# Performance work log

Measured on AMD Instinct MI355X. Metric: run time of the kernel, lower is better.

The kernel has to match this reference:

```python
import jax, jax.numpy as jnp
import numpy as np

DIM = 512
EPS = 1e-08
LN_EPS = 1e-05  # torch LayerNorm default


def layer_norm(x, g, b):
    mu = jnp.mean(x, axis=-1, keepdims=True)
    var = jnp.mean(jnp.square(x - mu), axis=-1, keepdims=True)
    return (x - mu) * jax.lax.rsqrt(var + LN_EPS) * g + b


def setup_inputs() -> dict:
    key = jax.random.key(0)
    ks = jax.random.split(key, 10)
    B, NQ, NK, D = 8, 1024, 2048, DIM
    s = 1.0 / np.sqrt(D)
    return {
        "inputs": jax.random.normal(ks[0], (B, NQ, D), jnp.float32),
        "context": jax.random.normal(ks[1], (B, NK, D), jnp.float32),
        "ln_in_g": jnp.ones((D,), jnp.float32),
        "ln_in_b": jnp.zeros((D,), jnp.float32),
        "ln_ctx_g": jnp.ones((D,), jnp.float32),
        "ln_ctx_b": jnp.zeros((D,), jnp.float32),
        "Wq": jax.random.uniform(ks[2], (D, D), jnp.float32, -s, s),
        "bq": jax.random.uniform(ks[3], (D,), jnp.float32, -s, s),
        "Wk": jax.random.uniform(ks[4], (D, D), jnp.float32, -s, s),
        "bk": jax.random.uniform(ks[5], (D,), jnp.float32, -s, s),
        "Wv": jax.random.uniform(ks[6], (D, D), jnp.float32, -s, s),
        "bv": jax.random.uniform(ks[7], (D,), jnp.float32, -s, s),
    }


def reference(inputs, context, ln_in_g, ln_in_b, ln_ctx_g, ln_ctx_b, Wq, bq, Wk, bk, Wv, bv):
    x = layer_norm(inputs, ln_in_g, ln_in_b)
    c = layer_norm(context, ln_ctx_g, ln_ctx_b)
    q = x @ Wq.T + bq  # [B, Nq, D]
    k = c @ Wk.T + bk  # [B, Nk, D]
    v = c @ Wv.T + bv  # [B, Nk, D]
    scale = DIM ** (-0.5)
    dots = jnp.einsum('bid,bjd->bij', q, k) * scale  # [B, Nq, Nk]
    attn = jax.nn.softmax(dots, axis=1) + EPS  # softmax over query axis
    attn = attn / jnp.sum(attn, axis=2, keepdims=True)  # renorm over key axis
    updates = jnp.einsum('bjd,bij->bid', v, attn)
    return updates
```

## Files before the change

kernel.cpp:

```cpp
#include <hip/hip_runtime.h>

using u16 = unsigned short;
typedef __attribute__((ext_vector_type(8))) short short8;
typedef __attribute__((ext_vector_type(4))) float floatx4;

#define NQ 1024
#define NK 2048
#define DD 512

__device__ __forceinline__ u16 f2bf(float f) {
  union { float f; unsigned u; } x; x.f = f;
  unsigned r = (x.u + 0x7fffu + ((x.u >> 16) & 1u)) >> 16;
  return (u16)r;
}
__device__ __forceinline__ float bf2f(u16 u) {
  union { unsigned u; float f; } x; x.u = ((unsigned)u) << 16; return x.f;
}
__device__ __forceinline__ float wave_sum(float v) {
#pragma unroll
  for (int off = 32; off > 0; off >>= 1) v += __shfl_down(v, off, 64);
  return v;
}
__device__ __forceinline__ void gload16(const u16* g, const u16* l) {
  __builtin_amdgcn_global_load_lds(
      (const __attribute__((address_space(1))) void*)g,
      (__attribute__((address_space(3))) void*)l, 16, 0, 0);
}

__global__ __launch_bounds__(256) void ln_prep(
    const float* __restrict__ X1, const float* __restrict__ G1,
    const float* __restrict__ B1, u16* __restrict__ Y1,
    const float* __restrict__ X2, const float* __restrict__ G2,
    const float* __restrict__ B2, u16* __restrict__ Y2,
    const float* __restrict__ Wq, const float* __restrict__ Wk,
    const float* __restrict__ Wv, u16* __restrict__ wqb,
    u16* __restrict__ wkb, u16* __restrict__ wvb, float* __restrict__ Zero) {
  const int bx = blockIdx.x;
  const int t = threadIdx.x;
  if (bx >= 6144) {
    int e = bx - 6144;
    if (e < 768) {
      const float* src = e < 256 ? Wq : (e < 512 ? Wk : Wv);
      u16* dst = e < 256 ? wqb : (e < 512 ? wkb : wvb);
      int i = ((e & 255) * 256 + t) * 4;
      float4 v = *(const float4*)(src + i);
      ushort4 o;
      o.x = f2bf(v.x); o.y = f2bf(v.y); o.z = f2bf(v.z); o.w = f2bf(v.w);
      *(ushort4*)(dst + i) = o;
    } else {
      int i = ((e - 768) * 256 + t) * 4;
      float4 z = {0.f, 0.f, 0.f, 0.f};
      *(float4*)(Zero + i) = z;
    }
    return;
  }
  const int wave = t >> 6, lane = t & 63;
  int row = bx * 4 + wave;
  const float *X, *G, *Bv; u16* Y;
  if (row < 8192) { X = X1; G = G1; Bv = B1; Y = Y1; }
  else { row -= 8192; X = X2; G = G2; Bv = B2; Y = Y2; }
  const float4* Xp = (const float4*)(X + (long)row * DD);
  float4 v0 = Xp[lane * 2], v1 = Xp[lane * 2 + 1];
  float s = v0.x + v0.y + v0.z + v0.w + v1.x + v1.y + v1.z + v1.w;
  float ss = v0.x * v0.x + v0.y * v0.y + v0.z * v0.z + v0.w * v0.w +
             v1.x * v1.x + v1.y * v1.y + v1.z * v1.z + v1.w * v1.w;
  s = wave_sum(s);  s = __shfl(s, 0, 64);
  ss = wave_sum(ss); ss = __shfl(ss, 0, 64);
  float mu = s * (1.f / DD);
  float var = ss * (1.f / DD) - mu * mu;
  float rs = rsqrtf(var + 1e-5f);
  const float4* Gp = (const float4*)G;
  const float4* Bp = (const float4*)Bv;
  float4 g0 = Gp[lane * 2], g1 = Gp[lane * 2 + 1];
  float4 b0 = Bp[lane * 2], b1 = Bp[lane * 2 + 1];
  short8 o;
  o[0] = (short)f2bf((v0.x - mu) * rs * g0.x + b0.x);
  o[1] = (short)f2bf((v0.y - mu) * rs * g0.y + b0.y);
  o[2] = (short)f2bf((v0.z - mu) * rs * g0.z + b0.z);
  o[3] = (short)f2bf((v0.w - mu) * rs * g0.w + b0.w);
  o[4] = (short)f2bf((v1.x - mu) * rs * g1.x + b1.x);
  o[5] = (short)f2bf((v1.y - mu) * rs * g1.y + b1.y);
  o[6] = (short)f2bf((v1.z - mu) * rs * g1.z + b1.z);
  o[7] = (short)f2bf((v1.w - mu) * rs * g1.w + b1.w);
  *(short8*)(Y + (long)row * DD + lane * 8) = o;
}

__global__ __launch_bounds__(256) void gemm_proj(
    const u16* __restrict__ A1, const u16* __restrict__ W1,
    const float* __restrict__ b1, u16* __restrict__ C1,
    const u16* __restrict__ A2, const u16* __restrict__ W2,
    const float* __restrict__ b2, u16* __restrict__ C2) {
  __shared__ u16 smem[16384];
  u16* lA = smem;
  u16* lB = smem + 8192;
  const u16 *A, *B; const float* bias; u16* Cout;
  int m0 = blockIdx.x * 128;
  if (blockIdx.x < 64) { A = A1; B = W1; bias = b1; Cout = C1; }
  else { A = A2; B = W2; bias = b2; Cout = C2; m0 = (blockIdx.x - 64) * 128; }
  const int n0 = blockIdx.y * 128;
  const int t = threadIdx.x, wave = t >> 6, lane = t & 63;
  const int fm = lane & 15, fq = lane >> 4;
  const int wm = (wave >> 1) * 64, wn = (wave & 1) * 64;

  const int srow = t >> 3;
  const int swz = ((t & 7) ^ (srow & 7)) * 8;
  const u16* gA = A + (long)(m0 + srow) * 512 + swz;
  const u16* gB = B + (long)(n0 + srow) * 512 + swz;
  u16* dA = lA + wave * 512;
  u16* dB = lB + wave * 512;

  floatx4 acc[4][4];
#pragma unroll
  for (int x = 0; x < 4; ++x)
#pragma unroll
    for (int y = 0; y < 4; ++y) { floatx4 z = {0.f, 0.f, 0.f, 0.f}; acc[x][y] = z; }

#pragma unroll 1
  for (int kt = 0; kt < 8; ++kt) {
    gload16(gA, dA);
    gload16(gA + 32L * 512, dA + 2048);
    gload16(gA + 64L * 512, dA + 4096);
    gload16(gA + 96L * 512, dA + 6144);
    gload16(gB, dB);
    gload16(gB + 32L * 512, dB + 2048);
    gload16(gB + 64L * 512, dB + 4096);
    gload16(gB + 96L * 512, dB + 6144);
    gA += 64; gB += 64;
    __syncthreads();
#pragma unroll
    for (int ks = 0; ks < 2; ++ks) {
      short8 af[4], bfr[4];
      const int csl = ((ks * 4 + fq) ^ (fm & 7)) * 8;
#pragma unroll
      for (int x = 0; x < 4; ++x)
        af[x] = *(const short8*)&lA[(wm + x * 16 + fm) * 64 + csl];
#pragma unroll
      for (int y = 0; y < 4; ++y)
        bfr[y] = *(const short8*)&lB[(wn + y * 16 + fm) * 64 + csl];
#pragma unroll
      for (int x = 0; x < 4; ++x)
#pragma unroll
        for (int y = 0; y < 4; ++y)
          acc[x][y] = __builtin_amdgcn_mfma_f32_16x16x32_bf16(af[x], bfr[y], acc[x][y], 0, 0, 0);
    }
    __syncthreads();
  }

  float bs[4];
#pragma unroll
  for (int y = 0; y < 4; ++y) bs[y] = bias[n0 + wn + y * 16 + fm];
#pragma unroll
  for (int x = 0; x < 4; ++x)
#pragma unroll
    for (int y = 0; y < 4; ++y) {
      const int cblk = (wn >> 4) + y;
#pragma unroll
      for (int r = 0; r < 4; ++r) {
        int rowl = wm + x * 16 + fq * 4 + r;
        smem[rowl * 128 + ((cblk ^ fq) * 16) + fm] = f2bf(acc[x][y][r] + bs[y]);
      }
    }
  __syncthreads();
#pragma unroll
  for (int p = 0; p < 8; ++p) {
    int rowl = p * 16 + (t >> 4);
    int c = t & 15;
    int q = (rowl >> 2) & 3;
    short8 v = *(const short8*)&smem[rowl * 128 + (((c >> 1) ^ q) * 16) + (c & 1) * 8];
    *(short8*)(Cout + (long)(m0 + rowl) * 512 + n0 + c * 8) = v;
  }
}

__global__ __launch_bounds__(256) void qk_vproj(
    const u16* __restrict__ qb, const u16* __restrict__ kb,
    u16* __restrict__ E, float* __restrict__ Z,
    const u16* __restrict__ wvb, const u16* __restrict__ cb,
    const float* __restrict__ bv, u16* __restrict__ vT,
    float* __restrict__ colV, float scale) {
  __shared__ u16 smem[16384];
  __shared__ float colred[128];
  u16* lA = smem;
  u16* lB = smem + 8192;

  const int bx = blockIdx.x;
  const bool is_qk = bx < 1024;
  const u16 *A, *B;
  int m0, n0, b;
  if (is_qk) {
    b = bx & 7;
    n0 = ((bx >> 3) & 15) * 128;
    m0 = (bx >> 7) * 128;
    A = qb + (long)b * (1024L * 512);
    B = kb + (long)b * (2048L * 512);
  } else {
    int e = bx - 1024;
    m0 = (e & 3) * 128;
    n0 = (e >> 2) * 128;
    b = 0;
    A = wvb;
    B = cb;
  }
  const int t = threadIdx.x, wave = t >> 6, lane = t & 63;
  const int fm = lane & 15, fq = lane >> 4;
  const int wm = (wave >> 1) * 64, wn = (wave & 1) * 64;

  const int srow = t >> 3;
  const int swz = ((t & 7) ^ (srow & 7)) * 8;
  const u16* gA = A + (long)(m0 + srow) * 512 + swz;
  const u16* gB = B + (long)(n0 + srow) * 512 + swz;
  u16* dA = lA + wave * 512;
  u16* dB = lB + wave * 512;

  floatx4 acc[4][4];
#pragma unroll
  for (int x = 0; x < 4; ++x)
#pragma unroll
    for (int y = 0; y < 4; ++y) { floatx4 z = {0.f, 0.f, 0.f, 0.f}; acc[x][y] = z; }

#pragma unroll 1
  for (int kt = 0; kt < 8; ++kt) {
    gload16(gA, dA);
    gload16(gA + 32L * 512, dA + 2048);
    gload16(gA + 64L * 512, dA + 4096);
    gload16(gA + 96L * 512, dA + 6144);
    gload16(gB, dB);
    gload16(gB + 32L * 512, dB + 2048);
    gload16(gB + 64L * 512, dB + 4096);
    gload16(gB + 96L * 512, dB + 6144);
    gA += 64; gB += 64;
    __syncthreads();
#pragma unroll
    for (int ks = 0; ks < 2; ++ks) {
      short8 af[4], bfr[4];
      const int csl = ((ks * 4 + fq) ^ (fm & 7)) * 8;
#pragma unroll
      for (int x = 0; x < 4; ++x)
        af[x] = *(const short8*)&lA[(wm + x * 16 + fm) * 64 + csl];
#pragma unroll
      for (int y = 0; y < 4; ++y)
        bfr[y] = *(const short8*)&lB[(wn + y * 16 + fm) * 64 + csl];
#pragma unroll
      for (int x = 0; x < 4; ++x)
#pragma unroll
        for (int y = 0; y < 4; ++y)
          acc[x][y] = __builtin_amdgcn_mfma_f32_16x16x32_bf16(af[x], bfr[y], acc[x][y], 0, 0, 0);
    }
    __syncthreads();
  }

  if (is_qk) {
    float s4[4] = {0.f, 0.f, 0.f, 0.f};
#pragma unroll
    for (int x = 0; x < 4; ++x)
#pragma unroll
      for (int y = 0; y < 4; ++y) {
        const int cblk = (wn >> 4) + y;
#pragma unroll
        for (int r = 0; r < 4; ++r) {
          int rowl = wm + x * 16 + fq * 4 + r;
          float e = __expf(acc[x][y][r] * scale);
          s4[y] += e;
          smem[rowl * 128 + ((cblk ^ fq) * 16) + fm] = f2bf(e);
        }
      }
#pragma unroll
    for (int y = 0; y < 4; ++y) {
      s4[y] += __shfl_xor(s4[y], 16, 64);
      s4[y] += __shfl_xor(s4[y], 32, 64);
    }
    if (t < 128) colred[t] = 0.f;
    __syncthreads();
    u16* Eg = E + (long)b * (1024L * 2048);
#pragma unroll
    for (int p = 0; p < 8; ++p) {
      int rowl = p * 16 + (t >> 4);
      int c = t & 15;
      int q = (rowl >> 2) & 3;
      short8 v = *(const short8*)&smem[rowl * 128 + (((c >> 1) ^ q) * 16) + (c & 1) * 8];
      *(short8*)(Eg + (long)(m0 + rowl) * 2048 + n0 + c * 8) = v;
    }
    if (fq == 0) {
#pragma unroll
      for (int y = 0; y < 4; ++y) atomicAdd(&colred[wn + y * 16 + fm], s4[y]);
    }
    __syncthreads();
    if (t < 128) atomicAdd(&Z[b * 2048 + n0 + t], colred[t]);
  } else {
    const int bb = n0 >> 11;
    const int j0c = n0 & 2047;
    float bsr[4][4];
#pragma unroll
    for (int x = 0; x < 4; ++x)
#pragma unroll
      for (int r = 0; r < 4; ++r)
        bsr[x][r] = bv[m0 + wm + x * 16 + fq * 4 + r];
    float rs[4][4];
#pragma unroll
    for (int x = 0; x < 4; ++x)
#pragma unroll
      for (int r = 0; r < 4; ++r) rs[x][r] = 0.f;
#pragma unroll
    for (int x = 0; x < 4; ++x)
#pragma unroll
      for (int y = 0; y < 4; ++y) {
        const int cblk = (wn >> 4) + y;
#pragma unroll
        for (int r = 0; r < 4; ++r) {
          int rowl = wm + x * 16 + fq * 4 + r;
          float val = acc[x][y][r] + bsr[x][r];
          rs[x][r] += val;
          smem[rowl * 128 + ((cblk ^ fq) * 16) + fm] = f2bf(val);
        }
      }
    __syncthreads();
    u16* Cg = vT + (long)bb * (512L * 2048) + j0c;
#pragma unroll
    for (int p = 0; p < 8; ++p) {
      int rowl = p * 16 + (t >> 4);
      int c = t & 15;
      int q = (rowl >> 2) & 3;
      short8 v = *(const short8*)&smem[rowl * 128 + (((c >> 1) ^ q) * 16) + (c & 1) * 8];
      *(short8*)(Cg + (long)(m0 + rowl) * 2048 + c * 8) = v;
    }
#pragma unroll
    for (int x = 0; x < 4; ++x)
#pragma unroll
      for (int r = 0; r < 4; ++r) {
        float s = rs[x][r];
        s += __shfl_xor(s, 1, 64);
        s += __shfl_xor(s, 2, 64);
        s += __shfl_xor(s, 4, 64);
        s += __shfl_xor(s, 8, 64);
        if (fm == 0)
          atomicAdd(&colV[bb * 512 + m0 + wm + x * 16 + fq * 4 + r], s);
      }
  }
}

__global__ __launch_bounds__(256) void scaleV(u16* __restrict__ vT,
                                              const float* __restrict__ Z) {
  const long f = ((long)blockIdx.x * 256 + threadIdx.x) * 8;
  const int b = (int)(f >> 20);
  const float* zp = Z + b * 2048 + (int)(f & 2047);
  short8 v = *(const short8*)(vT + f);
  short8 o;
#pragma unroll
  for (int k = 0; k < 8; ++k)
    o[k] = (short)f2bf(bf2f((u16)v[k]) * __builtin_amdgcn_rcpf(zp[k]));
  *(short8*)(vT + f) = o;
}

__global__ __launch_bounds__(256) void gemm_pv(const u16* __restrict__ E,
    const u16* __restrict__ V, const float* __restrict__ colV,
    const float* __restrict__ Z, float* __restrict__ out) {
  __shared__ u16 smem[8192];
  __shared__ u16 sZb[2048];
  u16* lA = smem;
  u16* lB = smem + 4096;
  const int id = blockIdx.x;
  const int b = id & 7;
  const int m0 = ((id >> 3) & 15) * 64, n0 = (id >> 7) * 64;
  const int t = threadIdx.x, wave = t >> 6, lane = t & 63;
  const int fm = lane & 15, fq = lane >> 4;
  const int wm = (wave >> 1) * 32, wn = (wave & 1) * 32;

  {
    int i = t * 8;
    float4 z0 = *(const float4*)(Z + b * 2048 + i);
    float4 z1 = *(const float4*)(Z + b * 2048 + i + 4);
    short8 o;
    o[0] = (short)f2bf(__builtin_amdgcn_rcpf(z0.x));
    o[1] = (short)f2bf(__builtin_amdgcn_rcpf(z0.y));
    o[2] = (short)f2bf(__builtin_amdgcn_rcpf(z0.z));
    o[3] = (short)f2bf(__builtin_amdgcn_rcpf(z0.w));
    o[4] = (short)f2bf(__builtin_amdgcn_rcpf(z1.x));
    o[5] = (short)f2bf(__builtin_amdgcn_rcpf(z1.y));
    o[6] = (short)f2bf(__builtin_amdgcn_rcpf(z1.z));
    o[7] = (short)f2bf(__builtin_amdgcn_rcpf(z1.w));
    *(short8*)&sZb[i] = o;
  }

  const int srow = t >> 3;
  const int swz = ((t & 7) ^ (srow & 7)) * 8;
  const u16* gA = E + (long)b * (1024L * 2048) + (long)(m0 + srow) * 2048 + swz;
  const u16* gB = V + (long)b * (512L * 2048) + (long)(n0 + srow) * 2048 + swz;
  u16* dA = lA + wave * 512;
  u16* dB = lB + wave * 512;

  floatx4 acc[2][2];
  floatx4 accR[2];
#pragma unroll
  for (int x = 0; x < 2; ++x) {
    floatx4 z = {0.f, 0.f, 0.f, 0.f};
    accR[x] = z;
#pragma unroll
    for (int y = 0; y < 2; ++y) acc[x][y] = z;
  }

#pragma unroll 1
  for (int kt = 0; kt < 32; ++kt) {
    gload16(gA, dA);
    gload16(gA + 32L * 2048, dA + 2048);
    gload16(gB, dB);
    gload16(gB + 32L * 2048, dB + 2048);
    gA += 64; gB += 64;
    __syncthreads();
#pragma unroll
    for (int ks = 0; ks < 2; ++ks) {
      short8 af[2], bfr[2];
      const int chunk = ks * 4 + fq;
      const int csl = (chunk ^ (fm & 7)) * 8;
#pragma unroll
      for (int x = 0; x < 2; ++x)
        af[x] = *(const short8*)&lA[(wm + x * 16 + fm) * 64 + csl];
#pragma unroll
      for (int y = 0; y < 2; ++y)
        bfr[y] = *(const short8*)&lB[(wn + y * 16 + fm) * 64 + csl];
      short8 zf = *(const short8*)&sZb[kt * 64 + chunk * 8];
#pragma unroll
      for (int x = 0; x < 2; ++x) {
#pragma unroll
        for (int y = 0; y < 2; ++y)
          acc[x][y] = __builtin_amdgcn_mfma_f32_16x16x32_bf16(af[x], bfr[y], acc[x][y], 0, 0, 0);
        accR[x] = __builtin_amdgcn_mfma_f32_16x16x32_bf16(af[x], zf, accR[x], 0, 0, 0);
      }
    }
    __syncthreads();
  }

  float cv[2];
#pragma unroll
  for (int y = 0; y < 2; ++y) cv[y] = colV[b * 512 + n0 + wn + y * 16 + fm];
  float* sO = (float*)smem;
#pragma unroll
  for (int x = 0; x < 2; ++x)
#pragma unroll
    for (int r = 0; r < 4; ++r) {
      float invR = __builtin_amdgcn_rcpf(accR[x][r] + 2048.f * 1e-8f);
      int rowl = wm + x * 16 + fq * 4 + r;
#pragma unroll
      for (int y = 0; y < 2; ++y) {
        const int cblk = (wn >> 4) + y;
        sO[rowl * 64 + ((cblk ^ fq) * 16) + fm] =
            (acc[x][y][r] + 1e-8f * cv[y]) * invR;
      }
    }
  __syncthreads();
  float* og = out + (long)b * (1024L * 512);
#pragma unroll
  for (int p = 0; p < 4; ++p) {
    int rowl = p * 16 + (t >> 4);
    int c = t & 15;
    int q = (rowl >> 2) & 3;
    float4 v = *(const float4*)&sO[rowl * 64 + (((c >> 2) ^ q) * 16) + (c & 3) * 4];
    *(float4*)(og + (long)(m0 + rowl) * 512 + n0 + c * 4) = v;
  }
}

extern "C" void kernel_launch(void* const* d_in, const int* in_sizes, int n_in,
                              void* d_out, int out_size, void* d_ws, size_t ws_size,
                              hipStream_t stream) {
  const float* inputs  = (const float*)d_in[0];
  const float* context = (const float*)d_in[1];
  const float* ln_in_g = (const float*)d_in[2];
  const float* ln_in_b = (const float*)d_in[3];
  const float* ln_ctx_g = (const float*)d_in[4];
  const float* ln_ctx_b = (const float*)d_in[5];
  const float* Wq = (const float*)d_in[6];
  const float* bq = (const float*)d_in[7];
  const float* Wk = (const float*)d_in[8];
  const float* bk = (const float*)d_in[9];
  const float* Wv = (const float*)d_in[10];
  const float* bv = (const float*)d_in[11];
  float* out = (float*)d_out;

  u16* ws = (u16*)d_ws;
  u16* xb  = ws;
  u16* qb  = xb + 8192L * 512;
  u16* cb  = qb + 8192L * 512;
  u16* wqb = cb + 16384L * 512;
  u16* wkb = wqb + 512L * 512;
  u16* wvb = wkb + 512L * 512;
  u16* kb  = wvb + 512L * 512;
  u16* vTs = kb + 16384L * 512;
  u16* E   = vTs + 8L * 512 * 2048;
  float* Z    = (float*)(E + 8L * 1024 * 2048);
  float* colV = Z + 8L * 2048;

  const float scale = 0.04419417382415922f;

  ln_prep<<<6932, 256, 0, stream>>>(inputs, ln_in_g, ln_in_b, xb,
                                    context, ln_ctx_g, ln_ctx_b, cb,
                                    Wq, Wk, Wv, wqb, wkb, wvb, Z);
  gemm_proj<<<dim3(192, 4, 1), 256, 0, stream>>>(xb, wqb, bq, qb,
                                                 cb, wkb, bk, kb);
  qk_vproj<<<1536, 256, 0, stream>>>(qb, kb, E, Z, wvb, cb, bv, vTs,
                                     colV, scale);
  scaleV<<<4096, 256, 0, stream>>>(vTs, Z);
  gemm_pv<<<1024, 256, 0, stream>>>(E, vTs, colV, Z, out);
}
```

Baseline: 215.1 us.

## Rewrite QK/V-projection GEMM as 256x256-tile 8-wave double-buffered pipelined kernel

The fused QK-exp and V-projection kernel moves from 128x128 tiles with 4 waves and a load-sync-compute loop to 256x256 tiles with 8 waves. It double-buffers 128KB of LDS and prefetches the next K-slice with global_load_lds while MFMAs run, using barriers and s_setprio to interleave. Block indices are remapped across XCDs. Larger tiles raise data reuse and the pipeline hides load latency, at the cost of far more LDS per block, fewer blocks (384) and heavier register use.

```diff
diff --git a/kernel.cpp b/kernel.cpp
--- a/kernel.cpp
+++ b/kernel.cpp
@@ -171,170 +171,205 @@
   }
 }
 
-__global__ __launch_bounds__(256) void qk_vproj(
+__global__ __launch_bounds__(512, 2) void qkvp8(
     const u16* __restrict__ qb, const u16* __restrict__ kb,
     u16* __restrict__ E, float* __restrict__ Z,
     const u16* __restrict__ wvb, const u16* __restrict__ cb,
     const float* __restrict__ bv, u16* __restrict__ vT,
     float* __restrict__ colV, float scale) {
-  __shared__ u16 smem[16384];
-  __shared__ float colred[128];
-  u16* lA = smem;
-  u16* lB = smem + 8192;
-
-  const int bx = blockIdx.x;
-  const bool is_qk = bx < 1024;
-  const u16 *A, *B;
+  __shared__ u16 ls[65536];
+  __shared__ float colred[256];
+
+  int bx = (int)blockIdx.x;
+  bx = (bx & 7) * 48 + (bx >> 3);
+  const bool is_qk = bx < 256;
+
+  const int t = threadIdx.x;
+  const int wave = t >> 6, lane = t & 63;
+  const int fm = lane & 15, fq = lane >> 4;
+  const int wr = wave >> 2, wc = wave & 3;
+  const int srow = t >> 3;
+  const int swz = ((t & 7) ^ (srow & 7)) * 8;
+
+  const u16 *Ap, *Bp;
   int m0, n0, b;
   if (is_qk) {
-    b = bx & 7;
-    n0 = ((bx >> 3) & 15) * 128;
-    m0 = (bx >> 7) * 128;
-    A = qb + (long)b * (1024L * 512);
-    B = kb + (long)b * (2048L * 512);
+    b = bx >> 5;
+    m0 = ((bx >> 3) & 3) * 256;
+    n0 = (bx & 7) * 256;
+    Ap = qb + (long)b * (1024L * 512);
+    Bp = kb + (long)b * (2048L * 512);
   } else {
-    int e = bx - 1024;
-    m0 = (e & 3) * 128;
-    n0 = (e >> 2) * 128;
-    b = 0;
-    A = wvb;
-    B = cb;
-  }
-  const int t = threadIdx.x, wave = t >> 6, lane = t & 63;
-  const int fm = lane & 15, fq = lane >> 4;
-  const int wm = (wave >> 1) * 64, wn = (wave & 1) * 64;
-
-  const int srow = t >> 3;
-  const int swz = ((t & 7) ^ (srow & 7)) * 8;
-  const u16* gA = A + (long)(m0 + srow) * 512 + swz;
-  const u16* gB = B + (long)(n0 + srow) * 512 + swz;
-  u16* dA = lA + wave * 512;
-  u16* dB = lB + wave * 512;
-
-  floatx4 acc[4][4];
-#pragma unroll
-  for (int x = 0; x < 4; ++x)
-#pragma unroll
-    for (int y = 0; y < 4; ++y) { floatx4 z = {0.f, 0.f, 0.f, 0.f}; acc[x][y] = z; }
+    int e = bx - 256;
+    m0 = (e & 1) * 256;
+    n0 = (e >> 1) * 256;
+    b = n0 >> 11;
+    Ap = wvb;
+    Bp = cb;
+  }
+
+  const u16* gAs = Ap + (long)(m0 + srow) * 512 + swz;
+  const u16* gBs = Bp + (long)(n0 + srow) * 512 + swz;
+  u16* dBase = ls + wave * 512;
+
+  auto stage = [&](const u16* gs, int par, int isB, int half, int tile) {
+    const u16* src = gs + (long)(half * 128) * 512 + tile * 64;
+    u16* d = dBase + par * 32768 + isB * 16384 + half * 8192;
+    gload16(src, d);
+    gload16(src + 64L * 512, d + 4096);
+  };
+
+  floatx4 acc[2][4][4];
+#pragma unroll
+  for (int mh = 0; mh < 2; ++mh)
+#pragma unroll
+    for (int x = 0; x < 4; ++x)
+#pragma unroll
+      for (int n = 0; n < 4; ++n) { floatx4 z = {0.f,0.f,0.f,0.f}; acc[mh][x][n] = z; }
+  short8 af[4][2], bf[2][2];
+
+  const int csl0 = (fq ^ (fm & 7)) * 8;
+  const int csl1 = ((4 + fq) ^ (fm & 7)) * 8;
+  const int aoff = wr * 8192 + fm * 64;
+  const int boff = 16384 + (wc >> 1) * 8192 + ((wc & 1) * 64 + fm) * 64;
+
+#define RDA(mh, par) { \
+  const u16* ab_ = ls + (par) * 32768 + aoff + (mh) * 4096; \
+  _Pragma("unroll") for (int x = 0; x < 4; ++x) { \
+    af[x][0] = *(const short8*)(ab_ + x * 1024 + csl0); \
+    af[x][1] = *(const short8*)(ab_ + x * 1024 + csl1); } }
+
+#define RDB(nh, par) { \
+  const u16* bb_ = ls + (par) * 32768 + boff + (nh) * 2048; \
+  _Pragma("unroll") for (int nn = 0; nn < 2; ++nn) { \
+    bf[nn][0] = *(const short8*)(bb_ + nn * 1024 + csl0); \
+    bf[nn][1] = *(const short8*)(bb_ + nn * 1024 + csl1); } }
+
+#define MM(mh, nh) { \
+  _Pragma("unroll") for (int x = 0; x < 4; ++x) \
+  _Pragma("unroll") for (int nn = 0; nn < 2; ++nn) { \
+    acc[mh][x][(nh)*2+nn] = __builtin_amdgcn_mfma_f32_16x16x32_bf16(af[x][0], bf[nn][0], acc[mh][x][(nh)*2+nn], 0, 0, 0); \
+    acc[mh][x][(nh)*2+nn] = __builtin_amdgcn_mfma_f32_16x16x32_bf16(af[x][1], bf[nn][1], acc[mh][x][(nh)*2+nn], 0, 0, 0); } }
+
+#define BARA __builtin_amdgcn_s_barrier(); \
+  asm volatile("s_waitcnt lgkmcnt(0)" ::: "memory"); \
+  __builtin_amdgcn_s_setprio(1)
+#define BARB __builtin_amdgcn_s_setprio(0); __builtin_amdgcn_s_barrier()
+
+  stage(gAs, 0, 0, 0, 0); stage(gAs, 0, 0, 1, 0);
+  stage(gBs, 0, 1, 0, 0); stage(gBs, 0, 1, 1, 0);
+  stage(gAs, 1, 0, 0, 1);
 
 #pragma unroll 1
-  for (int kt = 0; kt < 8; ++kt) {
-    gload16(gA, dA);
-    gload16(gA + 32L * 512, dA + 2048);
-    gload16(gA + 64L * 512, dA + 4096);
-    gload16(gA + 96L * 512, dA + 6144);
-    gload16(gB, dB);
-    gload16(gB + 32L * 512, dB + 2048);
-    gload16(gB + 64L * 512, dB + 4096);
-    gload16(gB + 96L * 512, dB + 6144);
-    gA += 64; gB += 64;
-    __syncthreads();
-#pragma unroll
-    for (int ks = 0; ks < 2; ++ks) {
-      short8 af[4], bfr[4];
-      const int csl = ((ks * 4 + fq) ^ (fm & 7)) * 8;
+  for (int i = 0; i < 4; ++i) {
+    const bool pf = i < 3;
+    const int t1 = 2 * i + 1, t2 = 2 * i + 2, t3 = 2 * i + 3;
+    asm volatile("s_waitcnt vmcnt(2)" ::: "memory");
+    RDA(0, 0); RDB(0, 0);
+    stage(gAs, 1, 0, 1, t1);
+    BARA; MM(0, 0); BARB;
+    RDB(1, 0);
+    stage(gBs, 1, 1, 0, t1);
+    BARA; MM(0, 1); BARB;
+    RDA(1, 0);
+    stage(gBs, 1, 1, 1, t1);
+    BARA; MM(1, 1); BARB;
+    RDB(0, 0);
+    if (pf) stage(gAs, 0, 0, 0, t2);
+    BARA; MM(1, 0); BARB;
+    if (pf) { asm volatile("s_waitcnt vmcnt(2)" ::: "memory"); }
+    else    { asm volatile("s_waitcnt vmcnt(0)" ::: "memory"); }
+    RDA(0, 1); RDB(0, 1);
+    if (pf) stage(gAs, 0, 0, 1, t2);
+    BARA; MM(0, 0); BARB;
+    RDB(1, 1);
+    if (pf) stage(gBs, 0, 1, 0, t2);
+    BARA; MM(0, 1); BARB;
+    RDA(1, 1);
+    if (pf) stage(gBs, 0, 1, 1, t2);
+    BARA; MM(1, 1); BARB;
+    RDB(0, 1);
+    if (pf) stage(gAs, 1, 0, 0, t3);
+    BARA; MM(1, 0); BARB;
+  }
+
+  if (is_qk) {
+    if (t < 256) colred[t] = 0.f;
+    float s4[4] = {0.f, 0.f, 0.f, 0.f};
+#pragma unroll
+    for (int mh = 0; mh < 2; ++mh)
 #pragma unroll
       for (int x = 0; x < 4; ++x)
-        af[x] = *(const short8*)&lA[(wm + x * 16 + fm) * 64 + csl];
-#pragma unroll
-      for (int y = 0; y < 4; ++y)
-        bfr[y] = *(const short8*)&lB[(wn + y * 16 + fm) * 64 + csl];
+#pragma unroll
+        for (int n = 0; n < 4; ++n) {
+          const int cblk = wc * 4 + n;
+          const int cs = ((cblk ^ fq) * 16) + fm;
+#pragma unroll
+          for (int r = 0; r < 4; ++r) {
+            float e = __expf(acc[mh][x][n][r] * scale);
+            s4[n] += e;
+            int row = wr * 128 + mh * 64 + x * 16 + fq * 4 + r;
+            ls[row * 256 + cs] = f2bf(e);
+          }
+        }
+    __syncthreads();
+#pragma unroll
+    for (int n = 0; n < 4; ++n) {
+      float s = s4[n];
+      s += __shfl_xor(s, 16, 64);
+      s += __shfl_xor(s, 32, 64);
+      if (fq == 0) atomicAdd(&colred[wc * 64 + n * 16 + fm], s);
+    }
+    u16* Eg = E + (long)b * (1024L * 2048) + (long)m0 * 2048 + n0;
+#pragma unroll
+    for (int p = 0; p < 16; ++p) {
+      int rowl = p * 16 + (t >> 5);
+      int c = t & 31;
+      int q = (rowl >> 2) & 3;
+      short8 v = *(const short8*)&ls[rowl * 256 + (((c >> 1) ^ q) * 16) + (c & 1) * 8];
+      *(short8*)(Eg + (long)rowl * 2048 + c * 8) = v;
+    }
+    __syncthreads();
+    if (t < 256) atomicAdd(&Z[b * 2048 + n0 + t], colred[t]);
+  } else {
+#pragma unroll
+    for (int mh = 0; mh < 2; ++mh)
 #pragma unroll
       for (int x = 0; x < 4; ++x)
 #pragma unroll
-        for (int y = 0; y < 4; ++y)
-          acc[x][y] = __builtin_amdgcn_mfma_f32_16x16x32_bf16(af[x], bfr[y], acc[x][y], 0, 0, 0);
-    }
-    __syncthreads();
-  }
-
-  if (is_qk) {
-    float s4[4] = {0.f, 0.f, 0.f, 0.f};
-#pragma unroll
-    for (int x = 0; x < 4; ++x)
-#pragma unroll
-      for (int y = 0; y < 4; ++y) {
-        const int cblk = (wn >> 4) + y;
-#pragma unroll
         for (int r = 0; r < 4; ++r) {
-          int rowl = wm + x * 16 + fq * 4 + r;
-          float e = __expf(acc[x][y][r] * scale);
-          s4[y] += e;
-          smem[rowl * 128 + ((cblk ^ fq) * 16) + fm] = f2bf(e);
+          int row = wr * 128 + mh * 64 + x * 16 + fq * 4 + r;
+          float bias = bv[m0 + row];
+          float rsum = 0.f;
+#pragma unroll
+          for (int n = 0; n < 4; ++n) {
+            const int cblk = wc * 4 + n;
+            float val = acc[mh][x][n][r] + bias;
+            rsum += val;
+            ls[row * 256 + ((cblk ^ fq) * 16) + fm] = f2bf(val);
+          }
+          rsum += __shfl_xor(rsum, 1, 64);
+          rsum += __shfl_xor(rsum, 2, 64);
+          rsum += __shfl_xor(rsum, 4, 64);
+          rsum += __shfl_xor(rsum, 8, 64);
+          if (fm == 0) atomicAdd(&colV[b * 512 + m0 + row], rsum);
         }
-      }
-#pragma unroll
-    for (int y = 0; y < 4; ++y) {
-      s4[y] += __shfl_xor(s4[y], 16, 64);
-      s4[y] += __shfl_xor(s4[y], 32, 64);
-    }
-    if (t < 128) colred[t] = 0.f;
-    __syncthreads();
-    u16* Eg = E + (long)b * (1024L * 2048);
-#pragma unroll
-    for (int p = 0; p < 8; ++p) {
-      int rowl = p * 16 + (t >> 4);
-      int c = t & 15;
+    __syncthreads();
+    u16* Vg = vT + (long)b * (512L * 2048) + (long)m0 * 2048 + (n0 & 2047);
+#pragma unroll
+    for (int p = 0; p < 16; ++p) {
+      int rowl = p * 16 + (t >> 5);
+      int c = t & 31;
       int q = (rowl >> 2) & 3;
-      short8 v = *(const short8*)&smem[rowl * 128 + (((c >> 1) ^ q) * 16) + (c & 1) * 8];
-      *(short8*)(Eg + (long)(m0 + rowl) * 2048 + n0 + c * 8) = v;
-    }
-    if (fq == 0) {
-#pragma unroll
-      for (int y = 0; y < 4; ++y) atomicAdd(&colred[wn + y * 16 + fm], s4[y]);
-    }
-    __syncthreads();
-    if (t < 128) atomicAdd(&Z[b * 2048 + n0 + t], colred[t]);
-  } else {
-    const int bb = n0 >> 11;
-    const int j0c = n0 & 2047;
-    float bsr[4][4];
-#pragma unroll
-    for (int x = 0; x < 4; ++x)
-#pragma unroll
-      for (int r = 0; r < 4; ++r)
-        bsr[x][r] = bv[m0 + wm + x * 16 + fq * 4 + r];
-    float rs[4][4];
-#pragma unroll
-    for (int x = 0; x < 4; ++x)
-#pragma unroll
-      for (int r = 0; r < 4; ++r) rs[x][r] = 0.f;
-#pragma unroll
-    for (int x = 0; x < 4; ++x)
-#pragma unroll
-      for (int y = 0; y < 4; ++y) {
-        const int cblk = (wn >> 4) + y;
-#pragma unroll
-        for (int r = 0; r < 4; ++r) {
-          int rowl = wm + x * 16 + fq * 4 + r;
-          float val = acc[x][y][r] + bsr[x][r];
-          rs[x][r] += val;
-          smem[rowl * 128 + ((cblk ^ fq) * 16) + fm] = f2bf(val);
-        }
-      }
-    __syncthreads();
-    u16* Cg = vT + (long)bb * (512L * 2048) + j0c;
-#pragma unroll
-    for (int p = 0; p < 8; ++p) {
-      int rowl = p * 16 + (t >> 4);
-      int c = t & 15;
-      int q = (rowl >> 2) & 3;
-      short8 v = *(const short8*)&smem[rowl * 128 + (((c >> 1) ^ q) * 16) + (c & 1) * 8];
-      *(short8*)(Cg + (long)(m0 + rowl) * 2048 + c * 8) = v;
-    }
-#pragma unroll
-    for (int x = 0; x < 4; ++x)
-#pragma unroll
-      for (int r = 0; r < 4; ++r) {
-        float s = rs[x][r];
-        s += __shfl_xor(s, 1, 64);
-        s += __shfl_xor(s, 2, 64);
-        s += __shfl_xor(s, 4, 64);
-        s += __shfl_xor(s, 8, 64);
-        if (fm == 0)
-          atomicAdd(&colV[bb * 512 + m0 + wm + x * 16 + fq * 4 + r], s);
-      }
-  }
+      short8 v = *(const short8*)&ls[rowl * 256 + (((c >> 1) ^ q) * 16) + (c & 1) * 8];
+      *(short8*)(Vg + (long)rowl * 2048 + c * 8) = v;
+    }
+  }
+#undef RDA
+#undef RDB
+#undef MM
+#undef BARA
+#undef BARB
 }
 
 __global__ __launch_bounds__(256) void scaleV(u16* __restrict__ vT,
@@ -494,8 +529,8 @@
                                     Wq, Wk, Wv, wqb, wkb, wvb, Z);
   gemm_proj<<<dim3(192, 4, 1), 256, 0, stream>>>(xb, wqb, bq, qb,
                                                  cb, wkb, bk, kb);
-  qk_vproj<<<1536, 256, 0, stream>>>(qb, kb, E, Z, wvb, cb, bv, vTs,
-                                     colV, scale);
+  qkvp8<<<384, 512, 0, stream>>>(qb, kb, E, Z, wvb, cb, bv, vTs,
+                                 colV, scale);
   scaleV<<<4096, 256, 0, stream>>>(vTs, Z);
   gemm_pv<<<1024, 256, 0, stream>>>(E, vTs, colV, Z, out);
 }
```

Measured after the change: 238.6 us. 10.9% more time.
